# Performance work log

Hardware: AMD Instinct MI355X
Metric: run time of the kernel (lower is better)

## Reference

```python
import jax, jax.numpy as jnp
import numpy as np

B, D, H, W, C = 2, 16, 16, 16, 64
CBAR = 32


def setup_inputs() -> dict:
    key = jax.random.key(0)
    ks = jax.random.split(key, 6)
    x = jax.random.normal(ks[0], (B, D, H, W, C), dtype=jnp.float32)
    # 1x1x1 Conv3D == per-voxel linear over channels; scale for stable softmax
    Wf = jax.random.normal(ks[1], (C, CBAR), dtype=jnp.float32) / np.sqrt(C)
    Wg = jax.random.normal(ks[2], (C, CBAR), dtype=jnp.float32) / np.sqrt(C)
    Wh = jax.random.normal(ks[3], (C, CBAR), dtype=jnp.float32) / np.sqrt(C)
    Wo = jax.random.normal(ks[4], (CBAR, C), dtype=jnp.float32) / np.sqrt(CBAR)
    bf = jnp.zeros((CBAR,), jnp.float32)
    bg = jnp.zeros((CBAR,), jnp.float32)
    bh = jnp.zeros((CBAR,), jnp.float32)
    bo = jnp.zeros((C,), jnp.float32)
    gamma = jnp.ones((), jnp.float32)
    return {"x": x, "Wf": Wf, "bf": bf, "Wg": Wg, "bg": bg,
            "Wh": Wh, "bh": bh, "Wo": Wo, "bo": bo, "gamma": gamma}


def reference(x, Wf, bf, Wg, bg, Wh, bh, Wo, bo, gamma):
    b, d, h, w, c = x.shape
    n = d * h * w
    xf = x.reshape(b, n, c)                       # [B, N, C]
    f = xf @ Wf + bf                              # [B, N, cbar] (keys)
    g = xf @ Wg + bg                              # [B, N, cbar] (queries)
    hv = xf @ Wh + bh                             # [B, N, cbar] (values)
    s = jnp.einsum('bqc,bkc->bqk', g, f)          # [B, N, N]
    beta = jax.nn.softmax(s, axis=-1)
    bhv = jnp.einsum('bqk,bkc->bqc', beta, hv)    # [B, N, cbar]
    o = bhv @ Wo + bo                             # [B, N, C]
    out = xf + gamma * o
    return out.reshape(b, d, h, w, c)
```

## Files before the change

### kernel.cpp

```cpp
#include <hip/hip_runtime.h>
#include <hip/hip_bf16.h>

typedef short short8 __attribute__((ext_vector_type(8)));
typedef float f32x4 __attribute__((ext_vector_type(4)));

__device__ __forceinline__ float bf2f(unsigned short v) {
    unsigned int u = ((unsigned int)v) << 16;
    float f;
    __builtin_memcpy(&f, &u, 4);
    return f;
}

__device__ __forceinline__ unsigned short f2bf(float f) {
    unsigned int u;
    __builtin_memcpy(&u, &f, 4);
    u += 0x7fffu + ((u >> 16) & 1u);
    return (unsigned short)(u >> 16);
}

__device__ __forceinline__ unsigned int pack2(float a, float b) {
    return (unsigned int)f2bf(a) | ((unsigned int)f2bf(b) << 16);
}

__device__ __forceinline__ void split2(float a, float b,
                                       unsigned int& hi, unsigned int& lo) {
    unsigned short ah = f2bf(a), bh = f2bf(b);
    float al = a - bf2f(ah), bl = b - bf2f(bh);
    hi = (unsigned int)ah | ((unsigned int)bh << 16);
    lo = (unsigned int)f2bf(al) | ((unsigned int)f2bf(bl) << 16);
}

__device__ __forceinline__ float loadv(const void* p, int idx, bool is_fp32) {
    return is_fp32 ? ((const float*)p)[idx] : bf2f(((const unsigned short*)p)[idx]);
}
__device__ __forceinline__ bool detect_fp32(const void* x, int tid, int* flag_sh) {
    if (tid < 64) {
        unsigned int w = ((const unsigned int*)x)[tid];
        unsigned int e = (w >> 7) & 0xFFu;
        unsigned long long m = __ballot(e > 140u);
        if (tid == 0) *flag_sh = (__popcll(m) >= 8) ? 1 : 0;
    }
    __syncthreads();
    return *flag_sh != 0;
}

__global__ __launch_bounds__(64) void proj_kernel(
    const void* __restrict__ x,
    const void* __restrict__ Wf, const void* __restrict__ bfv,
    const void* __restrict__ Wg, const void* __restrict__ bgv,
    const void* __restrict__ Wh, const void* __restrict__ bhv,
    unsigned short* __restrict__ F, unsigned short* __restrict__ G,
    unsigned short* __restrict__ Ht) {
    __shared__ int dflag;
    int lane = threadIdx.x;
    bool fp32 = detect_fp32(x, lane, &dflag);
    int Q = lane >> 4, l15 = lane & 15;
    int row0 = blockIdx.x << 4;

    short8 a0h, a0l, a1h, a1l;
    {
        int base = (row0 + l15) * 64 + Q * 8;
        union { unsigned int u[4]; short8 s8; } A0h, A0l, A1h, A1l;
        if (fp32) {
            const float* xf = (const float*)x;
            f32x4 v0 = *(const f32x4*)(xf + base);
            f32x4 v1 = *(const f32x4*)(xf + base + 4);
            f32x4 w0 = *(const f32x4*)(xf + base + 32);
            f32x4 w1 = *(const f32x4*)(xf + base + 36);
            split2(v0[0], v0[1], A0h.u[0], A0l.u[0]);
            split2(v0[2], v0[3], A0h.u[1], A0l.u[1]);
            split2(v1[0], v1[1], A0h.u[2], A0l.u[2]);
            split2(v1[2], v1[3], A0h.u[3], A0l.u[3]);
            split2(w0[0], w0[1], A1h.u[0], A1l.u[0]);
            split2(w0[2], w0[3], A1h.u[1], A1l.u[1]);
            split2(w1[0], w1[1], A1h.u[2], A1l.u[2]);
            split2(w1[2], w1[3], A1h.u[3], A1l.u[3]);
        } else {
            const unsigned short* xb = (const unsigned short*)x;
            A0h.s8 = *(const short8*)(xb + base);
            A1h.s8 = *(const short8*)(xb + base + 32);
            A0l.u[0] = A0l.u[1] = A0l.u[2] = A0l.u[3] = 0;
            A1l = A0l;
        }
        a0h = A0h.s8; a0l = A0l.s8; a1h = A1h.s8; a1l = A1l.s8;
    }

    const void* Ws[3] = {Wf, Wg, Wh};
    const void* bs[3] = {bfv, bgv, bhv};

#pragma unroll
    for (int m = 0; m < 3; m++) {
#pragma unroll
        for (int cb = 0; cb < 2; cb++) {
            union { unsigned int u[4]; short8 s8; } B0h, B0l, B1h, B1l;
#pragma unroll
            for (int jp = 0; jp < 4; jp++) {
                int k0 = Q * 8 + 2 * jp;
                float e0 = loadv(Ws[m], (k0 + 0) * 32 + cb * 16 + l15, fp32);
                float e1 = loadv(Ws[m], (k0 + 1) * 32 + cb * 16 + l15, fp32);
                split2(e0, e1, B0h.u[jp], B0l.u[jp]);
                float e2 = loadv(Ws[m], (k0 + 32) * 32 + cb * 16 + l15, fp32);
                float e3 = loadv(Ws[m], (k0 + 33) * 32 + cb * 16 + l15, fp32);
                split2(e2, e3, B1h.u[jp], B1l.u[jp]);
            }
            f32x4 z = {0.f, 0.f, 0.f, 0.f};
            f32x4 acc = __builtin_amdgcn_mfma_f32_16x16x32_bf16(a0h, B0h.s8, z, 0, 0, 0);
            acc = __builtin_amdgcn_mfma_f32_16x16x32_bf16(a0h, B0l.s8, acc, 0, 0, 0);
            acc = __builtin_amdgcn_mfma_f32_16x16x32_bf16(a0l, B0h.s8, acc, 0, 0, 0);
            acc = __builtin_amdgcn_mfma_f32_16x16x32_bf16(a1h, B1h.s8, acc, 0, 0, 0);
            acc = __builtin_amdgcn_mfma_f32_16x16x32_bf16(a1h, B1l.s8, acc, 0, 0, 0);
            acc = __builtin_amdgcn_mfma_f32_16x16x32_bf16(a1l, B1h.s8, acc, 0, 0, 0);
            float bias = loadv(bs[m], cb * 16 + l15, fp32);
            if (m < 2) {
                unsigned short* dst = (m == 0) ? F : G;
#pragma unroll
                for (int r = 0; r < 4; r++)
                    dst[(row0 + Q * 4 + r) * 32 + cb * 16 + l15] = f2bf(acc[r] + bias);
            } else {
                int b = row0 >> 12;
                int n0 = (row0 & 4095) + Q * 4;
                uint2 pk;
                pk.x = pack2(acc[0] + bias, acc[1] + bias);
                pk.y = pack2(acc[2] + bias, acc[3] + bias);
                *(uint2*)(Ht + b * 131072 + (cb * 16 + l15) * 4096 + n0) = pk;
            }
        }
    }
}

__global__ __launch_bounds__(512, 4) void attn_kernel(
    const unsigned short* __restrict__ F, const unsigned short* __restrict__ G,
    const unsigned short* __restrict__ Ht,
    const void* __restrict__ x,
    const void* __restrict__ Wo, const void* __restrict__ bo,
    const void* __restrict__ gamma_p,
    void* __restrict__ out) {
    __shared__ __attribute__((aligned(16))) unsigned short P_sh[8][2][16][40];
    __shared__ float O_lds[8][32][32];
    __shared__ float l_lds[8][32];
    __shared__ float Om[32][33];
    __shared__ float lmg[32];
    __shared__ float WoL[32][64];
    __shared__ float boL[64];
    __shared__ int dflag;

    int tid = threadIdx.x;
    bool fp32 = detect_fp32(x, tid, &dflag);

    for (int i = tid; i < 2048; i += 512) WoL[i >> 6][i & 63] = loadv(Wo, i, fp32);
    if (tid < 64) boL[tid] = loadv(bo, tid, fp32);

    int bx = blockIdx.x;
    int b = bx >> 7;
    int q0 = (bx & 127) << 5;
    int wave = tid >> 6;
    int lane = tid & 63;
    int Q = lane >> 4, l15 = lane & 15;

    const unsigned short* Fb = F + (b << 17);
    const unsigned short* Gb = G + (b << 17);
    const unsigned short* Htb = Ht + (b << 17);

    short8 g0 = *(const short8*)(Gb + ((q0 + l15) << 5) + (Q << 3));
    short8 g1 = *(const short8*)(Gb + ((q0 + 16 + l15) << 5) + (Q << 3));

    f32x4 O00 = {0.f, 0.f, 0.f, 0.f}, O01 = O00, O10 = O00, O11 = O00;
    float ls0 = 0.f, ls1 = 0.f;

    int k_begin = wave << 9;
    for (int it = 0; it < 16; ++it) {
        int kk = k_begin + (it << 5);
        short8 af0 = *(const short8*)(Fb + ((kk + l15) << 5) + (Q << 3));
        short8 af1 = *(const short8*)(Fb + ((kk + 16 + l15) << 5) + (Q << 3));
        short8 bh0 = *(const short8*)(Htb + (l15 << 12) + kk + (Q << 3));
        short8 bh1 = *(const short8*)(Htb + ((16 + l15) << 12) + kk + (Q << 3));

        f32x4 z = {0.f, 0.f, 0.f, 0.f};
        f32x4 c00 = __builtin_amdgcn_mfma_f32_16x16x32_bf16(af0, g0, z, 0, 0, 0);
        f32x4 c01 = __builtin_amdgcn_mfma_f32_16x16x32_bf16(af1, g0, z, 0, 0, 0);
        f32x4 c10 = __builtin_amdgcn_mfma_f32_16x16x32_bf16(af0, g1, z, 0, 0, 0);
        f32x4 c11 = __builtin_amdgcn_mfma_f32_16x16x32_bf16(af1, g1, z, 0, 0, 0);

        float e00[4], e01[4], e10[4], e11[4];
#pragma unroll
        for (int r = 0; r < 4; r++) {
            e00[r] = __expf(c00[r]); e01[r] = __expf(c01[r]);
            e10[r] = __expf(c10[r]); e11[r] = __expf(c11[r]);
            ls0 += e00[r] + e01[r];
            ls1 += e10[r] + e11[r];
        }

        uint2 w0, w1;
        w0.x = pack2(e00[0], e00[1]); w0.y = pack2(e00[2], e00[3]);
        w1.x = pack2(e01[0], e01[1]); w1.y = pack2(e01[2], e01[3]);
        *(uint2*)&P_sh[wave][0][l15][Q * 4] = w0;
        *(uint2*)&P_sh[wave][0][l15][16 + Q * 4] = w1;
        uint2 w2, w3;
        w2.x = pack2(e10[0], e10[1]); w2.y = pack2(e10[2], e10[3]);
        w3.x = pack2(e11[0], e11[1]); w3.y = pack2(e11[2], e11[3]);
        *(uint2*)&P_sh[wave][1][l15][Q * 4] = w2;
        *(uint2*)&P_sh[wave][1][l15][16 + Q * 4] = w3;

        short8 pf0 = *(const short8*)&P_sh[wave][0][l15][Q * 8];
        short8 pf1 = *(const short8*)&P_sh[wave][1][l15][Q * 8];

        O00 = __builtin_amdgcn_mfma_f32_16x16x32_bf16(pf0, bh0, O00, 0, 0, 0);
        O01 = __builtin_amdgcn_mfma_f32_16x16x32_bf16(pf0, bh1, O01, 0, 0, 0);
        O10 = __builtin_amdgcn_mfma_f32_16x16x32_bf16(pf1, bh0, O10, 0, 0, 0);
        O11 = __builtin_amdgcn_mfma_f32_16x16x32_bf16(pf1, bh1, O11, 0, 0, 0);
    }

    ls0 += __shfl_xor(ls0, 16); ls0 += __shfl_xor(ls0, 32);
    ls1 += __shfl_xor(ls1, 16); ls1 += __shfl_xor(ls1, 32);
    if (Q == 0) {
        l_lds[wave][l15] = ls0;
        l_lds[wave][16 + l15] = ls1;
    }
#pragma unroll
    for (int r = 0; r < 4; r++) {
        O_lds[wave][(Q << 2) | r][l15]            = O00[r];
        O_lds[wave][(Q << 2) | r][16 + l15]       = O01[r];
        O_lds[wave][16 + ((Q << 2) | r)][l15]     = O10[r];
        O_lds[wave][16 + ((Q << 2) | r)][16 + l15]= O11[r];
    }
    __syncthreads();

    if (tid < 32) {
        float s = 0.f;
#pragma unroll
        for (int w = 0; w < 8; w++) s += l_lds[w][tid];
        lmg[tid] = 1.0f / s;
    }
#pragma unroll
    for (int idx = tid; idx < 1024; idx += 512) {
        int q = idx >> 5, c = idx & 31;
        float s = 0.f;
#pragma unroll
        for (int w = 0; w < 8; w++) s += O_lds[w][q][c];
        Om[q][c] = s;
    }
    __syncthreads();

    int q = tid >> 4;
    int ch = (tid & 15) << 2;
    float a0 = 0.f, a1 = 0.f, a2 = 0.f, a3 = 0.f;
#pragma unroll
    for (int c = 0; c < 32; c++) {
        float ob = Om[q][c];
        f32x4 wr = *(const f32x4*)&WoL[c][ch];
        a0 += ob * wr[0]; a1 += ob * wr[1]; a2 += ob * wr[2]; a3 += ob * wr[3];
    }
    float inv = lmg[q];
    float gam = loadv(gamma_p, 0, fp32);
    int gq = q0 + q;
    int obase = (((b << 12) + gq) << 6) + ch;
    if (fp32) {
        f32x4 xv = *(const f32x4*)((const float*)x + obase);
        f32x4 ov;
        ov[0] = xv[0] + gam * (a0 * inv + boL[ch + 0]);
        ov[1] = xv[1] + gam * (a1 * inv + boL[ch + 1]);
        ov[2] = xv[2] + gam * (a2 * inv + boL[ch + 2]);
        ov[3] = xv[3] + gam * (a3 * inv + boL[ch + 3]);
        *(f32x4*)((float*)out + obase) = ov;
    } else {
        const unsigned short* xb = (const unsigned short*)x;
        unsigned short* ob16 = (unsigned short*)out;
        uint2 pk;
        pk.x = pack2(bf2f(xb[obase + 0]) + gam * (a0 * inv + boL[ch + 0]),
                     bf2f(xb[obase + 1]) + gam * (a1 * inv + boL[ch + 1]));
        pk.y = pack2(bf2f(xb[obase + 2]) + gam * (a2 * inv + boL[ch + 2]),
                     bf2f(xb[obase + 3]) + gam * (a3 * inv + boL[ch + 3]));
        *(uint2*)(ob16 + obase) = pk;
    }
}

extern "C" void kernel_launch(void* const* d_in, const int* in_sizes, int n_in,
                              void* d_out, int out_size, void* d_ws, size_t ws_size,
                              hipStream_t stream) {
    const void* x   = d_in[0];
    const void* Wf  = d_in[1];
    const void* bfv = d_in[2];
    const void* Wg  = d_in[3];
    const void* bgv = d_in[4];
    const void* Wh  = d_in[5];
    const void* bhv = d_in[6];
    const void* Wo  = d_in[7];
    const void* bo  = d_in[8];
    const void* gam = d_in[9];

    unsigned short* F  = (unsigned short*)d_ws;
    unsigned short* G  = F + 262144;
    unsigned short* Ht = G + 262144;

    proj_kernel<<<512, 64, 0, stream>>>(x, Wf, bfv, Wg, bgv, Wh, bhv, F, G, Ht);
    attn_kernel<<<256, 512, 0, stream>>>(F, G, Ht, x, Wo, bo, gam, d_out);
}
```

Baseline: 103.9 us.

## Stage projection weights in LDS, prefetch attention tiles, truncate P packing

The projection kernel now uses two waves per block. They cooperatively split the weights into bf16 hi/lo halves and store them in LDS, replacing the per-lane scattered global loads and repeated splitting. The attention loop software-prefetches the next iteration's F and Ht fragments into registers so that global latency overlaps the MFMA and exp work. P is packed to bf16 by truncation with a single perm instead of round-to-nearest, and attention launch bounds are relaxed from 4 to 2 blocks per CU, which allows more registers but may reduce occupancy. Truncation adds a small downward bias to the probabilities.

```diff
diff --git a/kernel.cpp b/kernel.cpp
--- a/kernel.cpp
+++ b/kernel.cpp
@@ -20,6 +20,13 @@
 
 __device__ __forceinline__ unsigned int pack2(float a, float b) {
     return (unsigned int)f2bf(a) | ((unsigned int)f2bf(b) << 16);
+}
+
+__device__ __forceinline__ unsigned int pack_trunc(float a, float b) {
+    unsigned int ua, ub;
+    __builtin_memcpy(&ua, &a, 4);
+    __builtin_memcpy(&ub, &b, 4);
+    return __builtin_amdgcn_perm(ub, ua, 0x07060302u);
 }
 
 __device__ __forceinline__ void split2(float a, float b,
@@ -44,18 +51,38 @@
     return *flag_sh != 0;
 }
 
-__global__ __launch_bounds__(64) void proj_kernel(
+__global__ __launch_bounds__(128) void proj_kernel(
     const void* __restrict__ x,
     const void* __restrict__ Wf, const void* __restrict__ bfv,
     const void* __restrict__ Wg, const void* __restrict__ bgv,
     const void* __restrict__ Wh, const void* __restrict__ bhv,
     unsigned short* __restrict__ F, unsigned short* __restrict__ G,
     unsigned short* __restrict__ Ht) {
+    __shared__ unsigned int WTh[3 * 32 * 36];
+    __shared__ unsigned int WTl[3 * 32 * 36];
+    __shared__ float bL[96];
     __shared__ int dflag;
-    int lane = threadIdx.x;
-    bool fp32 = detect_fp32(x, lane, &dflag);
+    int tid = threadIdx.x;
+    bool fp32 = detect_fp32(x, tid, &dflag);
+    int lane = tid & 63, wave = tid >> 6;
     int Q = lane >> 4, l15 = lane & 15;
-    int row0 = blockIdx.x << 4;
+    int row0 = (blockIdx.x * 2 + wave) << 4;
+
+    const void* Ws[3] = {Wf, Wg, Wh};
+    const void* bs[3] = {bfv, bgv, bhv};
+
+    for (int i = tid; i < 3072; i += 128) {
+        int m = i >> 10;
+        int r = i & 1023;
+        int p = r >> 5, n = r & 31;
+        float e0 = loadv(Ws[m], (2 * p) * 32 + n, fp32);
+        float e1 = loadv(Ws[m], (2 * p + 1) * 32 + n, fp32);
+        unsigned int hi, lo;
+        split2(e0, e1, hi, lo);
+        WTh[(m * 32 + n) * 36 + p] = hi;
+        WTl[(m * 32 + n) * 36 + p] = lo;
+    }
+    if (tid < 96) bL[tid] = loadv(bs[tid >> 5], tid & 31, fp32);
 
     short8 a0h, a0l, a1h, a1l;
     {
@@ -84,25 +111,18 @@
         }
         a0h = A0h.s8; a0l = A0l.s8; a1h = A1h.s8; a1l = A1l.s8;
     }
-
-    const void* Ws[3] = {Wf, Wg, Wh};
-    const void* bs[3] = {bfv, bgv, bhv};
+    __syncthreads();
 
 #pragma unroll
     for (int m = 0; m < 3; m++) {
 #pragma unroll
         for (int cb = 0; cb < 2; cb++) {
-            union { unsigned int u[4]; short8 s8; } B0h, B0l, B1h, B1l;
-#pragma unroll
-            for (int jp = 0; jp < 4; jp++) {
-                int k0 = Q * 8 + 2 * jp;
-                float e0 = loadv(Ws[m], (k0 + 0) * 32 + cb * 16 + l15, fp32);
-                float e1 = loadv(Ws[m], (k0 + 1) * 32 + cb * 16 + l15, fp32);
-                split2(e0, e1, B0h.u[jp], B0l.u[jp]);
-                float e2 = loadv(Ws[m], (k0 + 32) * 32 + cb * 16 + l15, fp32);
-                float e3 = loadv(Ws[m], (k0 + 33) * 32 + cb * 16 + l15, fp32);
-                split2(e2, e3, B1h.u[jp], B1l.u[jp]);
-            }
+            int rowbase = (m * 32 + cb * 16 + l15) * 36;
+            union { uint4 v; short8 s8; } B0h, B0l, B1h, B1l;
+            B0h.v = *(const uint4*)&WTh[rowbase + Q * 4];
+            B1h.v = *(const uint4*)&WTh[rowbase + 16 + Q * 4];
+            B0l.v = *(const uint4*)&WTl[rowbase + Q * 4];
+            B1l.v = *(const uint4*)&WTl[rowbase + 16 + Q * 4];
             f32x4 z = {0.f, 0.f, 0.f, 0.f};
             f32x4 acc = __builtin_amdgcn_mfma_f32_16x16x32_bf16(a0h, B0h.s8, z, 0, 0, 0);
             acc = __builtin_amdgcn_mfma_f32_16x16x32_bf16(a0h, B0l.s8, acc, 0, 0, 0);
@@ -110,7 +130,7 @@
             acc = __builtin_amdgcn_mfma_f32_16x16x32_bf16(a1h, B1h.s8, acc, 0, 0, 0);
             acc = __builtin_amdgcn_mfma_f32_16x16x32_bf16(a1h, B1l.s8, acc, 0, 0, 0);
             acc = __builtin_amdgcn_mfma_f32_16x16x32_bf16(a1l, B1h.s8, acc, 0, 0, 0);
-            float bias = loadv(bs[m], cb * 16 + l15, fp32);
+            float bias = bL[m * 32 + cb * 16 + l15];
             if (m < 2) {
                 unsigned short* dst = (m == 0) ? F : G;
 #pragma unroll
@@ -128,7 +148,7 @@
     }
 }
 
-__global__ __launch_bounds__(512, 4) void attn_kernel(
+__global__ __launch_bounds__(512, 2) void attn_kernel(
     const unsigned short* __restrict__ F, const unsigned short* __restrict__ G,
     const unsigned short* __restrict__ Ht,
     const void* __restrict__ x,
@@ -168,12 +188,18 @@
     float ls0 = 0.f, ls1 = 0.f;
 
     int k_begin = wave << 9;
+    short8 af0 = *(const short8*)(Fb + ((k_begin + l15) << 5) + (Q << 3));
+    short8 af1 = *(const short8*)(Fb + ((k_begin + 16 + l15) << 5) + (Q << 3));
+    short8 bh0 = *(const short8*)(Htb + (l15 << 12) + k_begin + (Q << 3));
+    short8 bh1 = *(const short8*)(Htb + ((16 + l15) << 12) + k_begin + (Q << 3));
+
     for (int it = 0; it < 16; ++it) {
-        int kk = k_begin + (it << 5);
-        short8 af0 = *(const short8*)(Fb + ((kk + l15) << 5) + (Q << 3));
-        short8 af1 = *(const short8*)(Fb + ((kk + 16 + l15) << 5) + (Q << 3));
-        short8 bh0 = *(const short8*)(Htb + (l15 << 12) + kk + (Q << 3));
-        short8 bh1 = *(const short8*)(Htb + ((16 + l15) << 12) + kk + (Q << 3));
+        int itn = (it < 15) ? it + 1 : 15;
+        int kn = k_begin + (itn << 5);
+        short8 naf0 = *(const short8*)(Fb + ((kn + l15) << 5) + (Q << 3));
+        short8 naf1 = *(const short8*)(Fb + ((kn + 16 + l15) << 5) + (Q << 3));
+        short8 nbh0 = *(const short8*)(Htb + (l15 << 12) + kn + (Q << 3));
+        short8 nbh1 = *(const short8*)(Htb + ((16 + l15) << 12) + kn + (Q << 3));
 
         f32x4 z = {0.f, 0.f, 0.f, 0.f};
         f32x4 c00 = __builtin_amdgcn_mfma_f32_16x16x32_bf16(af0, g0, z, 0, 0, 0);
@@ -191,13 +217,13 @@
         }
 
         uint2 w0, w1;
-        w0.x = pack2(e00[0], e00[1]); w0.y = pack2(e00[2], e00[3]);
-        w1.x = pack2(e01[0], e01[1]); w1.y = pack2(e01[2], e01[3]);
+        w0.x = pack_trunc(e00[0], e00[1]); w0.y = pack_trunc(e00[2], e00[3]);
+        w1.x = pack_trunc(e01[0], e01[1]); w1.y = pack_trunc(e01[2], e01[3]);
         *(uint2*)&P_sh[wave][0][l15][Q * 4] = w0;
         *(uint2*)&P_sh[wave][0][l15][16 + Q * 4] = w1;
         uint2 w2, w3;
-        w2.x = pack2(e10[0], e10[1]); w2.y = pack2(e10[2], e10[3]);
-        w3.x = pack2(e11[0], e11[1]); w3.y = pack2(e11[2], e11[3]);
+        w2.x = pack_trunc(e10[0], e10[1]); w2.y = pack_trunc(e10[2], e10[3]);
+        w3.x = pack_trunc(e11[0], e11[1]); w3.y = pack_trunc(e11[2], e11[3]);
         *(uint2*)&P_sh[wave][1][l15][Q * 4] = w2;
         *(uint2*)&P_sh[wave][1][l15][16 + Q * 4] = w3;
 
@@ -208,6 +234,8 @@
         O01 = __builtin_amdgcn_mfma_f32_16x16x32_bf16(pf0, bh1, O01, 0, 0, 0);
         O10 = __builtin_amdgcn_mfma_f32_16x16x32_bf16(pf1, bh0, O10, 0, 0, 0);
         O11 = __builtin_amdgcn_mfma_f32_16x16x32_bf16(pf1, bh1, O11, 0, 0, 0);
+
+        af0 = naf0; af1 = naf1; bh0 = nbh0; bh1 = nbh1;
     }
 
     ls0 += __shfl_xor(ls0, 16); ls0 += __shfl_xor(ls0, 32);
@@ -218,10 +246,10 @@
     }
 #pragma unroll
     for (int r = 0; r < 4; r++) {
-        O_lds[wave][(Q << 2) | r][l15]            = O00[r];
-        O_lds[wave][(Q << 2) | r][16 + l15]       = O01[r];
-        O_lds[wave][16 + ((Q << 2) | r)][l15]     = O10[r];
-        O_lds[wave][16 + ((Q << 2) | r)][16 + l15]= O11[r];
+        O_lds[wave][(Q << 2) | r][l15]             = O00[r];
+        O_lds[wave][(Q << 2) | r][16 + l15]        = O01[r];
+        O_lds[wave][16 + ((Q << 2) | r)][l15]      = O10[r];
+        O_lds[wave][16 + ((Q << 2) | r)][16 + l15] = O11[r];
     }
     __syncthreads();
 
@@ -292,6 +320,6 @@
     unsigned short* G  = F + 262144;
     unsigned short* Ht = G + 262144;
 
-    proj_kernel<<<512, 64, 0, stream>>>(x, Wf, bfv, Wg, bgv, Wh, bhv, F, G, Ht);
+    proj_kernel<<<256, 128, 0, stream>>>(x, Wf, bfv, Wg, bgv, Wh, bhv, F, G, Ht);
     attn_kernel<<<256, 512, 0, stream>>>(F, G, Ht, x, Wo, bo, gam, d_out);
 }
```

Result: faster. 99.25 us (-4.4%).
